# Optimization experiments

Measured on AMD Instinct MI355X. Metric: run time of the kernel, lower is better.

## Reference

```python
import jax, jax.numpy as jnp
import numpy as np
import math

BN_EPS = 1e-5
L2_EPS = 1e-12
TEMPARATURE = 0.01
Q_IN_DIM = 256


def _masked_bn(y, mask, gamma, beta):
    # y: [S, L, D], mask: [S, L] float (1 = valid packed row).
    # Emulates BatchNorm1d (training mode) over the packed valid rows.
    m = mask[..., None]
    cnt = jnp.sum(mask)
    mean = jnp.sum(y * m, axis=(0, 1)) / cnt
    var = jnp.sum(jnp.square(y - mean) * m, axis=(0, 1)) / cnt  # biased var
    return (y - mean) * jax.lax.rsqrt(var + BN_EPS) * gamma + beta


def _ctx_proj(x, W, b, gamma, beta, mask, normalize):
    y = jnp.einsum('sld,od->slo', x, W) + b
    y = jax.nn.relu(_masked_bn(y, mask, gamma, beta))
    if normalize:
        n = jnp.linalg.norm(y, axis=-1, keepdims=True)
        y = y / jnp.maximum(n, L2_EPS)
    return y


def setup_inputs() -> dict:
    key = jax.random.key(0)
    ks = jax.random.split(key, 8)
    S, La, Lb = 256, 128, 512
    Dq, Dkv, Dqk, Dv = 256, 265, 512, 512
    A = jax.random.normal(ks[0], (S, La, Dq), jnp.float32)
    B = jax.random.normal(ks[1], (S, Lb, Dkv), jnp.float32)
    a_lens = jax.random.randint(ks[2], (S,), 1, La + 1, jnp.int32)
    b_lens = jax.random.randint(ks[3], (S,), 1, Lb + 1, jnp.int32)
    pk = jax.random.split(ks[4], 4)
    sc = 0.05
    return {
        'A': A, 'B': B, 'a_lens': a_lens, 'b_lens': b_lens,
        'Wq': sc * jax.random.normal(pk[0], (Dqk, Dq), jnp.float32),
        'bq': jnp.zeros((Dqk,), jnp.float32),
        'gq': jnp.ones((Dqk,), jnp.float32),
        'betaq': jnp.zeros((Dqk,), jnp.float32),
        'Wk': sc * jax.random.normal(pk[1], (Dqk, Dkv), jnp.float32),
        'bk': jnp.zeros((Dqk,), jnp.float32),
        'gk': jnp.ones((Dqk,), jnp.float32),
        'betak': jnp.zeros((Dqk,), jnp.float32),
        'Wv': sc * jax.random.normal(pk[2], (Dv, Dkv), jnp.float32),
        'bv': jnp.zeros((Dv,), jnp.float32),
        'gv': jnp.ones((Dv,), jnp.float32),
        'betav': jnp.zeros((Dv,), jnp.float32),
        'Wf': sc * jax.random.normal(pk[3], (Dq, Dv), jnp.float32),
        'bf': jnp.zeros((Dq,), jnp.float32),
        'gf': jnp.ones((Dq,), jnp.float32),
        'betaf': jnp.zeros((Dq,), jnp.float32),
    }


def reference(A, B, a_lens, b_lens,
              Wq, bq, gq, betaq,
              Wk, bk, gk, betak,
              Wv, bv, gv, betav,
              Wf, bf, gf, betaf):
    S, La, _ = A.shape
    Lb = B.shape[1]
    mask_a = (jnp.arange(La)[None, :] < a_lens[:, None]).astype(A.dtype)  # [S, La]
    mask_b = (jnp.arange(Lb)[None, :] < b_lens[:, None]).astype(B.dtype)  # [S, Lb]

    q = _ctx_proj(A, Wq, bq, gq, betaq, mask_a, True)   # [S, La, Dqk]
    k = _ctx_proj(B, Wk, bk, gk, betak, mask_b, True)   # [S, Lb, Dqk]
    v = _ctx_proj(B, Wv, bv, gv, betav, mask_b, True)   # [S, Lb, Dv]

    scaler = 1.0 / (TEMPARATURE * math.sqrt(Q_IN_DIM))
    scores = jnp.einsum('sad,sbd->sab', q, k) * scaler  # [S, La, Lb]
    scores = jnp.where(mask_b[:, None, :] > 0, scores, -1e30)
    w = jax.nn.softmax(scores, axis=-1)
    wv = jnp.einsum('sab,sbd->sad', w, v)               # [S, La, Dv]

    f = _ctx_proj(wv, Wf, bf, gf, betaf, mask_a, False)  # [S, La, Dq]
    return f * mask_a[..., None]
```

## Files before the change

### kernel.cpp

```cpp
#include <hip/hip_runtime.h>
#include <hip/hip_bf16.h>
#include <stdint.h>


typedef __attribute__((ext_vector_type(8))) short short8;
typedef __attribute__((ext_vector_type(4))) float floatx4;

__device__ __forceinline__ float bf2f(short h) {
    union { unsigned u; float f; } c;
    c.u = ((unsigned)(unsigned short)h) << 16;
    return c.f;
}
__device__ __forceinline__ short f2bf(float f) {
    union { float f; unsigned u; } c;
    c.f = f;
    unsigned u = c.u + 0x7fffu + ((c.u >> 16) & 1u);
    return (short)(u >> 16);
}

__device__ __forceinline__ void async_cp16(const short* g, short* l) {
    __builtin_amdgcn_global_load_lds(
        (const __attribute__((address_space(1))) unsigned int*)g,
        (__attribute__((address_space(3))) unsigned int*)l, 16, 0, 0);
}

__device__ __forceinline__ short8 cvt8load(const float* p) {
    float4 f0 = *(const float4*)(p);
    float4 f1 = *(const float4*)(p + 4);
    short8 r;
    r[0] = f2bf(f0.x); r[1] = f2bf(f0.y); r[2] = f2bf(f0.z); r[3] = f2bf(f0.w);
    r[4] = f2bf(f1.x); r[5] = f2bf(f1.y); r[6] = f2bf(f1.z); r[7] = f2bf(f1.w);
    return r;
}
__device__ __forceinline__ short8 cvt8guard(const float* row, int c0, int Kin) {
    short8 r;
#pragma unroll
    for (int j = 0; j < 8; j++) {
        int c = c0 + j;
        r[j] = (c < Kin) ? f2bf(row[c]) : (short)0;
    }
    return r;
}

__global__ __launch_bounds__(256) void cvt_pad(const float* __restrict__ in,
                                               short* __restrict__ out,
                                               int kin, int kout) {
    long row = blockIdx.x;
    const float* src = in + row * (long)kin;
    short* dst = out + row * (long)kout;
    for (int c = threadIdx.x; c < kout; c += 256)
        dst[c] = (c < kin) ? f2bf(src[c]) : (short)0;
}

__global__ __launch_bounds__(256, 2)
void gemm256(const short* __restrict__ X,
             const short* __restrict__ W0, const short* __restrict__ W1,
             const float* __restrict__ bias0, const float* __restrict__ bias1,
             short* __restrict__ Y0, short* __restrict__ Y1,
             float* __restrict__ st0, float* __restrict__ st1,
             int N, int Kp, const int* __restrict__ lens, int Lshift,
             int nShift, int dual)
{
    __shared__ short SH[(256 + 128) * 96];
    short* At = SH;
    short* Bt = SH + 256 * 96;
    const int lin = blockIdx.x;
    const int xcd = lin & 7, sl = lin >> 3;
    const int nb = sl & ((1 << nShift) - 1);
    const int ms = sl >> nShift;
    const int m0 = (ms * 8 + xcd) * 256;
    int g = 0, n0;
    if (dual) { g = nb & 1; n0 = (nb >> 1) * 128; } else { n0 = nb * 128; }
    const short* W    = g ? W1 : W0;
    const float* bias = g ? bias1 : bias0;
    short* Y          = g ? Y1 : Y0;
    float* stats      = g ? st1 : st0;

    const int tid = threadIdx.x;
    const int l = tid & 63, w = tid >> 6;
    const int quad = l >> 4, l15 = l & 15;
    const int mo = w * 64;

    floatx4 acc[4][8];
#pragma unroll
    for (int i = 0; i < 4; i++)
#pragma unroll
        for (int j = 0; j < 8; j++) acc[i][j] = (floatx4){0.f, 0.f, 0.f, 0.f};

    int offA[12], offB[6];
#pragma unroll
    for (int c = 0; c < 12; c++) {
        unsigned e = c * 2048u + (unsigned)tid * 8u;
        unsigned row = e / 96u;
        unsigned col = e - row * 96u;
        offA[c] = (int)((unsigned)(m0 + row) * (unsigned)Kp + col);
    }
#pragma unroll
    for (int c = 0; c < 6; c++) {
        unsigned e = c * 2048u + (unsigned)tid * 8u;
        unsigned row = e / 96u;
        unsigned col = e - row * 96u;
        offB[c] = (int)((unsigned)(n0 + row) * (unsigned)Kp + col);
    }

    for (int k0 = 0; k0 < Kp; k0 += 96) {
        __syncthreads();
#pragma unroll
        for (int c = 0; c < 12; c++)
            async_cp16(X + offA[c] + k0, At + c * 2048 + tid * 8);
#pragma unroll
        for (int c = 0; c < 6; c++)
            async_cp16(W + offB[c] + k0, Bt + c * 2048 + tid * 8);
        __syncthreads();
#pragma unroll
        for (int seg = 0; seg < 3; seg++) {
            short8 af[4], bfr[8];
#pragma unroll
            for (int i = 0; i < 4; i++)
                af[i] = *(const short8*)(At + (mo + i * 16 + l15) * 96 + seg * 32 + quad * 8);
#pragma unroll
            for (int j = 0; j < 8; j++)
                bfr[j] = *(const short8*)(Bt + (j * 16 + l15) * 96 + seg * 32 + quad * 8);
#pragma unroll
            for (int i = 0; i < 4; i++)
#pragma unroll
                for (int j = 0; j < 8; j++)
                    acc[i][j] = __builtin_amdgcn_mfma_f32_16x16x32_bf16(af[i], bfr[j], acc[i][j], 0, 0, 0);
        }
    }

    __syncthreads();
    const int Lmask = (1 << Lshift) - 1;
    float msk[4][4];
#pragma unroll
    for (int i = 0; i < 4; i++)
#pragma unroll
        for (int r = 0; r < 4; r++) {
            int rg = m0 + mo + i * 16 + quad * 4 + r;
            msk[i][r] = ((rg & Lmask) < lens[rg >> Lshift]) ? 1.f : 0.f;
        }
    short* Cs = SH;
#pragma unroll
    for (int j = 0; j < 8; j++) {
        int coll = j * 16 + l15;
        float bv = bias[n0 + coll];
        float ps = 0.f, pss = 0.f;
#pragma unroll
        for (int i = 0; i < 4; i++)
#pragma unroll
            for (int r = 0; r < 4; r++) {
                int rl = mo + i * 16 + quad * 4 + r;
                float v = acc[i][j][r] + bv;
                Cs[rl * 132 + coll] = f2bf(v);
                ps += v * msk[i][r];
                pss += v * v * msk[i][r];
            }
        ps  += __shfl_xor(ps, 16, 64);  ps  += __shfl_xor(ps, 32, 64);
        pss += __shfl_xor(pss, 16, 64); pss += __shfl_xor(pss, 32, 64);
        if (l < 16) {
            atomicAdd(&stats[n0 + coll], ps);
            atomicAdd(&stats[N + n0 + coll], pss);
        }
    }
    __syncthreads();
#pragma unroll
    for (int c = 0; c < 16; c++) {
        int e = c * 2048 + tid * 8;
        int row = e >> 7, col = e & 127;
        short8 vv = *(const short8*)(Cs + row * 132 + col);
        *(short8*)(Y + (long)(m0 + row) * N + n0 + col) = vv;
    }
}

template<bool XBF16, bool KAL>
__global__ __launch_bounds__(256, 2)
void gemm_bt(const void* __restrict__ Xp, const float* __restrict__ W,
             const float* __restrict__ bias, short* __restrict__ Y,
             int N, int Kin, int Kp, float* __restrict__ stats,
             const int* __restrict__ lens, int Lshift)
{
    __shared__ short At[128 * 32];
    __shared__ short Bt[128 * 32];
    const int m0 = blockIdx.x * 128;
    const int n0 = blockIdx.y * 128;
    const int tid = threadIdx.x;
    const int w = tid >> 6, l = tid & 63;
    const int quad = l >> 4, l15 = l & 15;
    const int mo = (w & 1) * 64, no = (w >> 1) * 64;

    floatx4 acc[4][4];
#pragma unroll
    for (int i = 0; i < 4; i++)
#pragma unroll
        for (int j = 0; j < 4; j++) acc[i][j] = (floatx4){0.f, 0.f, 0.f, 0.f};

    const int srow = tid >> 2;
    const int sc8 = (tid & 3) * 8;

    for (int k0 = 0; k0 < Kp; k0 += 32) {
        __syncthreads();
        const int c0 = k0 + sc8;
        short8 a0, a1, b0, b1;
        if (XBF16) {
            const short* X = (const short*)Xp;
            a0 = *(const short8*)(X + (long)(m0 + srow) * Kp + c0);
            a1 = *(const short8*)(X + (long)(m0 + 64 + srow) * Kp + c0);
        } else {
            const float* X = (const float*)Xp;
            if (KAL) {
                a0 = cvt8load(X + (long)(m0 + srow) * Kin + c0);
                a1 = cvt8load(X + (long)(m0 + 64 + srow) * Kin + c0);
            } else {
                a0 = cvt8guard(X + (long)(m0 + srow) * Kin, c0, Kin);
                a1 = cvt8guard(X + (long)(m0 + 64 + srow) * Kin, c0, Kin);
            }
        }
        if (KAL) {
            b0 = cvt8load(W + (long)(n0 + srow) * Kin + c0);
            b1 = cvt8load(W + (long)(n0 + 64 + srow) * Kin + c0);
        } else {
            b0 = cvt8guard(W + (long)(n0 + srow) * Kin, c0, Kin);
            b1 = cvt8guard(W + (long)(n0 + 64 + srow) * Kin, c0, Kin);
        }
        *(short8*)(At + srow * 32 + sc8) = a0;
        *(short8*)(At + (64 + srow) * 32 + sc8) = a1;
        *(short8*)(Bt + srow * 32 + sc8) = b0;
        *(short8*)(Bt + (64 + srow) * 32 + sc8) = b1;
        __syncthreads();
        short8 af[4], bfr[4];
#pragma unroll
        for (int i = 0; i < 4; i++) {
            af[i]  = *(const short8*)(At + (mo + i * 16 + l15) * 32 + quad * 8);
            bfr[i] = *(const short8*)(Bt + (no + i * 16 + l15) * 32 + quad * 8);
        }
#pragma unroll
        for (int i = 0; i < 4; i++)
#pragma unroll
            for (int j = 0; j < 4; j++)
                acc[i][j] = __builtin_amdgcn_mfma_f32_16x16x32_bf16(af[i], bfr[j], acc[i][j], 0, 0, 0);
    }

    const int Lmask = (1 << Lshift) - 1;
    float msk[4][4];
#pragma unroll
    for (int i = 0; i < 4; i++)
#pragma unroll
        for (int r = 0; r < 4; r++) {
            int rg = m0 + mo + i * 16 + quad * 4 + r;
            msk[i][r] = ((rg & Lmask) < lens[rg >> Lshift]) ? 1.f : 0.f;
        }
#pragma unroll
    for (int j = 0; j < 4; j++) {
        int colj = n0 + no + j * 16 + l15;
        float bv = bias[colj];
        float ps = 0.f, pss = 0.f;
#pragma unroll
        for (int i = 0; i < 4; i++)
#pragma unroll
            for (int r = 0; r < 4; r++) {
                int rg = m0 + mo + i * 16 + quad * 4 + r;
                float v = acc[i][j][r] + bv;
                Y[(long)rg * N + colj] = f2bf(v);
                ps += v * msk[i][r];
                pss += v * v * msk[i][r];
            }
        ps  += __shfl_xor(ps, 16, 64);  ps  += __shfl_xor(ps, 32, 64);
        pss += __shfl_xor(pss, 16, 64); pss += __shfl_xor(pss, 32, 64);
        if (l < 16) {
            atomicAdd(&stats[colj], ps);
            atomicAdd(&stats[N + colj], pss);
        }
    }
}

__global__ void finalize_stats(float* __restrict__ stats, const float* __restrict__ g,
                               const float* __restrict__ beta,
                               const int* __restrict__ lens, int C)
{
    __shared__ int lred[256];
    int t = threadIdx.x;
    if (t < 256) lred[t] = lens[t];
    __syncthreads();
    for (int s2 = 128; s2 > 0; s2 >>= 1) {
        if (t < s2) lred[t] += lred[t + s2];
        __syncthreads();
    }
    float cnt = (float)lred[0];
    if (t < C) {
        float mean = stats[t] / cnt;
        float var = fmaxf(stats[C + t] / cnt - mean * mean, 0.f);
        float a = rsqrtf(var + 1e-5f) * g[t];
        stats[t] = a;
        stats[C + t] = beta[t] - mean * a;
    }
}

__global__ __launch_bounds__(256)
void apply_norm512(short* __restrict__ Y, const float* __restrict__ stats)
{
    int w = threadIdx.x >> 6, l = threadIdx.x & 63;
    long row = (long)blockIdx.x * 4 + w;
    short8 yv = *(const short8*)(Y + row * 512 + l * 8);
    float v[8];
    float ss = 0.f;
#pragma unroll
    for (int i = 0; i < 8; i++) {
        int c = l * 8 + i;
        float t = fmaxf(bf2f(yv[i]) * stats[c] + stats[512 + c], 0.f);
        v[i] = t;
        ss += t * t;
    }
#pragma unroll
    for (int off = 1; off < 64; off <<= 1) ss += __shfl_xor(ss, off, 64);
    float scl = 1.f / fmaxf(sqrtf(ss), 1e-12f);
    short8 o;
#pragma unroll
    for (int i = 0; i < 8; i++) o[i] = f2bf(v[i] * scl);
    *(short8*)(Y + row * 512 + l * 8) = o;
}

__global__ __launch_bounds__(256)
void attention(const short* __restrict__ q, const short* __restrict__ k,
               const short* __restrict__ v, const int* __restrict__ b_lens,
               short* __restrict__ wv, int wvStride)
{
    __shared__ short tile[32 * 520];
    __shared__ short Pscr[4][16 * 40];
    const int lin = blockIdx.x;
    const int xcd = lin & 7, sl = lin >> 3;
    const int a0 = (sl & 1) * 64;
    const int s = (sl >> 1) * 8 + xcd;
    const int tid = threadIdx.x;
    const int w = tid >> 6, l = tid & 63;
    const int quad = l >> 4, l15 = l & 15;
    const int blen = b_lens[s];
    const int sr = tid >> 3;
    const int scg = (tid & 7) * 8;

    short8 qf[16];
    const short* qbase = q + ((long)(s * 128 + a0 + w * 16 + l15)) * 512 + quad * 8;
#pragma unroll
    for (int kk = 0; kk < 16; kk++) qf[kk] = *(const short8*)(qbase + kk * 32);

    floatx4 sc[32];
#pragma unroll
    for (int i = 0; i < 32; i++) sc[i] = (floatx4){0.f, 0.f, 0.f, 0.f};

    const short* kbase = k + (long)s * 512 * 512;
    for (int bt2 = 0; bt2 < 16; ++bt2) {
        __syncthreads();
        const short* krow = kbase + (long)(bt2 * 32 + sr) * 512;
#pragma unroll
        for (int i = 0; i < 2; i++) {
            short8 t0 = *(const short8*)(krow + i * 256 + scg);
            short8 t1 = *(const short8*)(krow + i * 256 + 64 + scg);
            short8 t2 = *(const short8*)(krow + i * 256 + 128 + scg);
            short8 t3 = *(const short8*)(krow + i * 256 + 192 + scg);
            *(short8*)(&tile[sr * 520 + i * 256 + scg]) = t0;
            *(short8*)(&tile[sr * 520 + i * 256 + 64 + scg]) = t1;
            *(short8*)(&tile[sr * 520 + i * 256 + 128 + scg]) = t2;
            *(short8*)(&tile[sr * 520 + i * 256 + 192 + scg]) = t3;
        }
        __syncthreads();
#pragma unroll
        for (int kk = 0; kk < 16; kk++) {
            short8 f0 = *(const short8*)(&tile[l15 * 520 + kk * 32 + quad * 8]);
            short8 f1 = *(const short8*)(&tile[(16 + l15) * 520 + kk * 32 + quad * 8]);
            sc[bt2 * 2]     = __builtin_amdgcn_mfma_f32_16x16x32_bf16(qf[kk], f0, sc[bt2 * 2], 0, 0, 0);
            sc[bt2 * 2 + 1] = __builtin_amdgcn_mfma_f32_16x16x32_bf16(qf[kk], f1, sc[bt2 * 2 + 1], 0, 0, 0);
        }
    }

    const float scaler = 6.25f;
    float mrow[4] = {-__builtin_inff(), -__builtin_inff(), -__builtin_inff(), -__builtin_inff()};
#pragma unroll
    for (int bt = 0; bt < 32; ++bt) {
        bool valid = (bt * 16 + l15) < blen;
#pragma unroll
        for (int r = 0; r < 4; r++) {
            float v2 = valid ? sc[bt][r] * scaler : -__builtin_inff();
            sc[bt][r] = v2;
            mrow[r] = fmaxf(mrow[r], v2);
        }
    }
#pragma unroll
    for (int r = 0; r < 4; r++) {
#pragma unroll
        for (int off = 1; off < 16; off <<= 1)
            mrow[r] = fmaxf(mrow[r], __shfl_xor(mrow[r], off, 64));
    }
    float ssum[4] = {0.f, 0.f, 0.f, 0.f};
#pragma unroll
    for (int bt = 0; bt < 32; ++bt)
#pragma unroll
        for (int r = 0; r < 4; r++) {
            float p = __expf(sc[bt][r] - mrow[r]);
            sc[bt][r] = p;
            ssum[r] += p;
        }
#pragma unroll
    for (int r = 0; r < 4; r++) {
#pragma unroll
        for (int off = 1; off < 16; off <<= 1) ssum[r] += __shfl_xor(ssum[r], off, 64);
        ssum[r] = 1.f / ssum[r];
    }

    short8 pf[16];
    short* Pw = Pscr[w];
#pragma unroll
    for (int kk = 0; kk < 16; kk++) {
#pragma unroll
        for (int half = 0; half < 2; half++)
#pragma unroll
            for (int r = 0; r < 4; r++)
                Pw[(quad * 4 + r) * 40 + half * 16 + l15] = f2bf(sc[kk * 2 + half][r] * ssum[r]);
        pf[kk] = *(const short8*)(&Pw[l15 * 40 + quad * 8]);
    }

    const short* vbase = v + (long)s * 512 * 512;
    short* wvbase = wv + (long)(s * 128 + a0 + w * 16 + quad * 4) * wvStride;
    for (int dt = 0; dt < 16; ++dt) {
        __syncthreads();
#pragma unroll
        for (int round = 0; round < 2; round++) {
            int b = round * 256 + tid;
            const short* vr = vbase + (long)b * 512 + dt * 32;
            short8 x0 = *(const short8*)(vr);
            short8 x1 = *(const short8*)(vr + 8);
            short8 x2 = *(const short8*)(vr + 16);
            short8 x3 = *(const short8*)(vr + 24);
#pragma unroll
            for (int j = 0; j < 8; j++) {
                tile[j * 520 + b]        = x0[j];
                tile[(8 + j) * 520 + b]  = x1[j];
                tile[(16 + j) * 520 + b] = x2[j];
                tile[(24 + j) * 520 + b] = x3[j];
            }
        }
        __syncthreads();
        floatx4 o0 = (floatx4){0.f, 0.f, 0.f, 0.f};
        floatx4 o1 = (floatx4){0.f, 0.f, 0.f, 0.f};
#pragma unroll
        for (int kk = 0; kk < 16; kk++) {
            short8 f0 = *(const short8*)(&tile[l15 * 520 + kk * 32 + quad * 8]);
            short8 f1 = *(const short8*)(&tile[(16 + l15) * 520 + kk * 32 + quad * 8]);
            o0 = __builtin_amdgcn_mfma_f32_16x16x32_bf16(pf[kk], f0, o0, 0, 0, 0);
            o1 = __builtin_amdgcn_mfma_f32_16x16x32_bf16(pf[kk], f1, o1, 0, 0, 0);
        }
#pragma unroll
        for (int r = 0; r < 4; r++) {
            wvbase[(long)r * wvStride + dt * 32 + l15]      = f2bf(o0[r]);
            wvbase[(long)r * wvStride + dt * 32 + 16 + l15] = f2bf(o1[r]);
        }
    }

    if (wvStride > 512) {
        int r = tid >> 2, cb = (tid & 3) * 16;
        short8 z = (short8){0, 0, 0, 0, 0, 0, 0, 0};
        short* pz = wv + (long)(s * 128 + a0 + r) * wvStride + 512 + cb;
        *(short8*)(pz) = z;
        *(short8*)(pz + 8) = z;
    }
}

__global__ __launch_bounds__(256)
void apply_f(const short* __restrict__ Yf, const float* __restrict__ stats,
             const int* __restrict__ a_lens, float* __restrict__ out)
{
    const long total = (long)32768 * 256;
    for (long e = (long)blockIdx.x * 256 + threadIdx.x; e < total; e += (long)gridDim.x * 256) {
        int c = (int)(e & 255);
        long row = e >> 8;
        int sI = (int)(row >> 7), pos = (int)(row & 127);
        float v = fmaxf(bf2f(Yf[e]) * stats[c] + stats[256 + c], 0.f);
        out[e] = (pos < a_lens[sI]) ? v : 0.f;
    }
}

extern "C" void kernel_launch(void* const* d_in, const int* in_sizes, int n_in,
                              void* d_out, int out_size, void* d_ws, size_t ws_size,
                              hipStream_t stream)
{
    (void)in_sizes; (void)n_in; (void)out_size;
    const float* A     = (const float*)d_in[0];
    const float* B     = (const float*)d_in[1];
    const int* a_lens  = (const int*)d_in[2];
    const int* b_lens  = (const int*)d_in[3];
    const float* Wq    = (const float*)d_in[4];
    const float* bq    = (const float*)d_in[5];
    const float* gq    = (const float*)d_in[6];
    const float* betaq = (const float*)d_in[7];
    const float* Wk    = (const float*)d_in[8];
    const float* bk    = (const float*)d_in[9];
    const float* gk    = (const float*)d_in[10];
    const float* betak = (const float*)d_in[11];
    const float* Wv    = (const float*)d_in[12];
    const float* bv    = (const float*)d_in[13];
    const float* gv    = (const float*)d_in[14];
    const float* betav = (const float*)d_in[15];
    const float* Wf    = (const float*)d_in[16];
    const float* bfp   = (const float*)d_in[17];
    const float* gf    = (const float*)d_in[18];
    const float* betaf = (const float*)d_in[19];
    float* out = (float*)d_out;
    char* base = (char*)d_ws;

    const size_t oWqb = 0;
    const size_t oWkb = oWqb + 294912;
    const size_t oWvb = oWkb + 294912;
    const size_t oWfb = oWvb + 294912;
    const size_t oBbf = oWfb + 294912;
    const size_t oQb  = oBbf + 75497472;
    const size_t oYv  = oQb + 33554432;
    const size_t oKb  = oYv + 134217728;
    const size_t oSt  = oKb + 134217728;
    const size_t FAST_NEED = oSt + 16384;

    if (ws_size >= FAST_NEED) {
        short* Wqb = (short*)(base + oWqb);
        short* Wkb = (short*)(base + oWkb);
        short* Wvb = (short*)(base + oWvb);
        short* Wfb = (short*)(base + oWfb);
        short* Bbf = (short*)(base + oBbf);
        short* qb  = (short*)(base + oQb);
        short* Yv  = (short*)(base + oYv);
        short* kb  = (short*)(base + oKb);
        short* Abf = (short*)(base + oKb);
        short* wvb = (short*)(base + oBbf);
        short* Yf  = (short*)(base + oQb);
        float* stQ = (float*)(base + oSt);
        float* stK = stQ + 1024;
        float* stV = stQ + 2048;
        float* stF = stQ + 3072;

        hipMemsetAsync(stQ, 0, 16384, stream);

        cvt_pad<<<32768, 256, 0, stream>>>(A, Abf, 256, 288);
        cvt_pad<<<131072, 256, 0, stream>>>(B, Bbf, 265, 288);
        cvt_pad<<<512, 256, 0, stream>>>(Wq, Wqb, 256, 288);
        cvt_pad<<<512, 256, 0, stream>>>(Wk, Wkb, 265, 288);
        cvt_pad<<<512, 256, 0, stream>>>(Wv, Wvb, 265, 288);
        cvt_pad<<<256, 256, 0, stream>>>(Wf, Wfb, 512, 576);

        gemm256<<<512, 256, 0, stream>>>(
            Abf, Wqb, Wqb, bq, bq, qb, qb, stQ, stQ, 512, 288, a_lens, 7, 2, 0);
        gemm256<<<4096, 256, 0, stream>>>(
            Bbf, Wvb, Wkb, bv, bk, Yv, kb, stV, stK, 512, 288, b_lens, 9, 3, 1);

        finalize_stats<<<1, 512, 0, stream>>>(stV, gv, betav, b_lens, 512);
        finalize_stats<<<1, 512, 0, stream>>>(stK, gk, betak, b_lens, 512);
        finalize_stats<<<1, 512, 0, stream>>>(stQ, gq, betaq, a_lens, 512);
        apply_norm512<<<32768, 256, 0, stream>>>(Yv, stV);
        apply_norm512<<<32768, 256, 0, stream>>>(kb, stK);
        apply_norm512<<<8192, 256, 0, stream>>>(qb, stQ);

        attention<<<512, 256, 0, stream>>>(qb, kb, Yv, b_lens, wvb, 576);

        gemm256<<<256, 256, 0, stream>>>(
            wvb, Wfb, Wfb, bfp, bfp, Yf, Yf, stF, stF, 256, 576, a_lens, 7, 1, 0);
        finalize_stats<<<1, 512, 0, stream>>>(stF, gf, betaf, a_lens, 256);
        apply_f<<<8192, 256, 0, stream>>>(Yf, stF, a_lens, out);
        return;
    }

    short* qb  = (short*)(base);
    short* Yv  = (short*)(base + 33554432);
    short* kb  = (short*)(base + 33554432 + 134217728);
    short* wvb = (short*)(base + 33554432 + 2L * 134217728);
    float* stQ = (float*)(base + 2L * 33554432 + 2L * 134217728);
    float* stK = stQ + 1024;
    float* stV = stQ + 2048;
    float* stF = stQ + 3072;
    short* Yf  = qb;

    hipMemsetAsync(stQ, 0, 16384, stream);

    gemm_bt<false, true><<<dim3(256, 4), 256, 0, stream>>>(
        A, Wq, bq, qb, 512, 256, 256, stQ, a_lens, 7);
    gemm_bt<false, false><<<dim3(1024, 4), 256, 0, stream>>>(
        B, Wv, bv, Yv, 512, 265, 288, stV, b_lens, 9);
    finalize_stats<<<1, 512, 0, stream>>>(stV, gv, betav, b_lens, 512);
    apply_norm512<<<32768, 256, 0, stream>>>(Yv, stV);
    gemm_bt<false, false><<<dim3(1024, 4), 256, 0, stream>>>(
        B, Wk, bk, kb, 512, 265, 288, stK, b_lens, 9);
    finalize_stats<<<1, 512, 0, stream>>>(stK, gk, betak, b_lens, 512);
    apply_norm512<<<32768, 256, 0, stream>>>(kb, stK);
    finalize_stats<<<1, 512, 0, stream>>>(stQ, gq, betaq, a_lens, 512);
    apply_norm512<<<8192, 256, 0, stream>>>(qb, stQ);
    attention<<<512, 256, 0, stream>>>(qb, kb, Yv, b_lens, wvb, 512);
    gemm_bt<true, true><<<dim3(256, 2), 256, 0, stream>>>(
        wvb, Wf, bfp, Yf, 256, 512, 512, stF, a_lens, 7);
    finalize_stats<<<1, 512, 0, stream>>>(stF, gf, betaf, a_lens, 256);
    apply_f<<<8192, 256, 0, stream>>>(Yf, stF, a_lens, out);
}
```

Before: 857.1 us.

## Double-buffer gemm256 K-loop with 32-wide stages and two-pass epilogue staging

Replaces the single-buffered 96-wide K tile loop in gemm256 with a double-buffered 32-wide pipeline, so async global-to-LDS loads for the next step are issued while MFMAs run on the current buffer, with one barrier per step. Shared memory shrinks from 384x96 to 24576 shorts, which may help occupancy. Because the smaller LDS cannot hold the full 256x128 output tile, the epilogue now writes it in two 128-row passes through LDS. The trade-off is more loop iterations and barriers, plus extra synchronisation in the epilogue.

Result: no change. 859.3 us (+0.2%).

```diff
diff --git a/kernel.cpp b/kernel.cpp
--- a/kernel.cpp
+++ b/kernel.cpp
@@ -61,9 +61,7 @@
              int N, int Kp, const int* __restrict__ lens, int Lshift,
              int nShift, int dual)
 {
-    __shared__ short SH[(256 + 128) * 96];
-    short* At = SH;
-    short* Bt = SH + 256 * 96;
+    __shared__ short SH[24576];
     const int lin = blockIdx.x;
     const int xcd = lin & 7, sl = lin >> 3;
     const int nb = sl & ((1 << nShift) - 1);
@@ -87,49 +85,57 @@
 #pragma unroll
         for (int j = 0; j < 8; j++) acc[i][j] = (floatx4){0.f, 0.f, 0.f, 0.f};
 
-    int offA[12], offB[6];
-#pragma unroll
-    for (int c = 0; c < 12; c++) {
-        unsigned e = c * 2048u + (unsigned)tid * 8u;
-        unsigned row = e / 96u;
-        unsigned col = e - row * 96u;
-        offA[c] = (int)((unsigned)(m0 + row) * (unsigned)Kp + col);
-    }
-#pragma unroll
-    for (int c = 0; c < 6; c++) {
-        unsigned e = c * 2048u + (unsigned)tid * 8u;
-        unsigned row = e / 96u;
-        unsigned col = e - row * 96u;
-        offB[c] = (int)((unsigned)(n0 + row) * (unsigned)Kp + col);
-    }
-
-    for (int k0 = 0; k0 < Kp; k0 += 96) {
-        __syncthreads();
-#pragma unroll
-        for (int c = 0; c < 12; c++)
-            async_cp16(X + offA[c] + k0, At + c * 2048 + tid * 8);
-#pragma unroll
-        for (int c = 0; c < 6; c++)
-            async_cp16(W + offB[c] + k0, Bt + c * 2048 + tid * 8);
-        __syncthreads();
-#pragma unroll
-        for (int seg = 0; seg < 3; seg++) {
-            short8 af[4], bfr[8];
-#pragma unroll
-            for (int i = 0; i < 4; i++)
-                af[i] = *(const short8*)(At + (mo + i * 16 + l15) * 96 + seg * 32 + quad * 8);
+    const int srow = tid >> 2;
+    const int scol = (tid & 3) * 8;
+    const short* Xs = X + (long)(m0 + srow) * Kp + scol;
+    const short* Ws = W + (long)(n0 + srow) * Kp + scol;
+    const long strideA = (long)64 * Kp;
+    const int nsteps = Kp >> 5;
+
+    {
+        short* At = SH;
+        short* Bt = SH + 8192;
+#pragma unroll
+        for (int c = 0; c < 4; c++)
+            async_cp16(Xs + c * strideA, At + c * 2048 + tid * 8);
+#pragma unroll
+        for (int c = 0; c < 2; c++)
+            async_cp16(Ws + c * strideA, Bt + c * 2048 + tid * 8);
+    }
+    __syncthreads();
+
+    int cur = 0;
+    for (int t = 0; t < nsteps; t++) {
+        if (t + 1 < nsteps) {
+            short* At = SH + (cur ^ 1) * 12288;
+            short* Bt = At + 8192;
+            const short* Xk = Xs + (t + 1) * 32;
+            const short* Wk = Ws + (t + 1) * 32;
+#pragma unroll
+            for (int c = 0; c < 4; c++)
+                async_cp16(Xk + c * strideA, At + c * 2048 + tid * 8);
+#pragma unroll
+            for (int c = 0; c < 2; c++)
+                async_cp16(Wk + c * strideA, Bt + c * 2048 + tid * 8);
+        }
+        const short* At = SH + cur * 12288;
+        const short* Bt = At + 8192;
+        short8 af[4], bfr[8];
+#pragma unroll
+        for (int i = 0; i < 4; i++)
+            af[i] = *(const short8*)(At + (mo + i * 16 + l15) * 32 + quad * 8);
+#pragma unroll
+        for (int j = 0; j < 8; j++)
+            bfr[j] = *(const short8*)(Bt + (j * 16 + l15) * 32 + quad * 8);
+#pragma unroll
+        for (int i = 0; i < 4; i++)
 #pragma unroll
             for (int j = 0; j < 8; j++)
-                bfr[j] = *(const short8*)(Bt + (j * 16 + l15) * 96 + seg * 32 + quad * 8);
-#pragma unroll
-            for (int i = 0; i < 4; i++)
-#pragma unroll
-                for (int j = 0; j < 8; j++)
-                    acc[i][j] = __builtin_amdgcn_mfma_f32_16x16x32_bf16(af[i], bfr[j], acc[i][j], 0, 0, 0);
-        }
-    }
-
-    __syncthreads();
+                acc[i][j] = __builtin_amdgcn_mfma_f32_16x16x32_bf16(af[i], bfr[j], acc[i][j], 0, 0, 0);
+        __syncthreads();
+        cur ^= 1;
+    }
+
     const int Lmask = (1 << Lshift) - 1;
     float msk[4][4];
 #pragma unroll
@@ -139,36 +145,52 @@
             int rg = m0 + mo + i * 16 + quad * 4 + r;
             msk[i][r] = ((rg & Lmask) < lens[rg >> Lshift]) ? 1.f : 0.f;
         }
-    short* Cs = SH;
+    float bv[8];
+#pragma unroll
+    for (int j = 0; j < 8; j++) bv[j] = bias[n0 + j * 16 + l15];
+
 #pragma unroll
     for (int j = 0; j < 8; j++) {
-        int coll = j * 16 + l15;
-        float bv = bias[n0 + coll];
         float ps = 0.f, pss = 0.f;
 #pragma unroll
         for (int i = 0; i < 4; i++)
 #pragma unroll
             for (int r = 0; r < 4; r++) {
-                int rl = mo + i * 16 + quad * 4 + r;
-                float v = acc[i][j][r] + bv;
-                Cs[rl * 132 + coll] = f2bf(v);
+                float v = acc[i][j][r] + bv[j];
                 ps += v * msk[i][r];
                 pss += v * v * msk[i][r];
             }
         ps  += __shfl_xor(ps, 16, 64);  ps  += __shfl_xor(ps, 32, 64);
         pss += __shfl_xor(pss, 16, 64); pss += __shfl_xor(pss, 32, 64);
         if (l < 16) {
-            atomicAdd(&stats[n0 + coll], ps);
-            atomicAdd(&stats[N + n0 + coll], pss);
-        }
-    }
-    __syncthreads();
-#pragma unroll
-    for (int c = 0; c < 16; c++) {
-        int e = c * 2048 + tid * 8;
-        int row = e >> 7, col = e & 127;
-        short8 vv = *(const short8*)(Cs + row * 132 + col);
-        *(short8*)(Y + (long)(m0 + row) * N + n0 + col) = vv;
+            atomicAdd(&stats[n0 + j * 16 + l15], ps);
+            atomicAdd(&stats[N + n0 + j * 16 + l15], pss);
+        }
+    }
+
+    short* Cs = SH;
+#pragma unroll
+    for (int pass = 0; pass < 2; pass++) {
+        __syncthreads();
+        if ((w >> 1) == pass) {
+            const int mol = (w & 1) * 64;
+#pragma unroll
+            for (int j = 0; j < 8; j++)
+#pragma unroll
+                for (int i = 0; i < 4; i++)
+#pragma unroll
+                    for (int r = 0; r < 4; r++)
+                        Cs[(mol + i * 16 + quad * 4 + r) * 132 + j * 16 + l15] =
+                            f2bf(acc[i][j][r] + bv[j]);
+        }
+        __syncthreads();
+#pragma unroll
+        for (int c = 0; c < 8; c++) {
+            int e = c * 2048 + tid * 8;
+            int row = e >> 7, col = e & 127;
+            short8 vv = *(const short8*)(Cs + row * 132 + col);
+            *(short8*)(Y + (long)(m0 + pass * 128 + row) * N + n0 + col) = vv;
+        }
     }
 }
 
@@ -252,14 +274,14 @@
 #pragma unroll
     for (int j = 0; j < 4; j++) {
         int colj = n0 + no + j * 16 + l15;
-        float bv = bias[colj];
+        float bvs = bias[colj];
         float ps = 0.f, pss = 0.f;
 #pragma unroll
         for (int i = 0; i < 4; i++)
 #pragma unroll
             for (int r = 0; r < 4; r++) {
                 int rg = m0 + mo + i * 16 + quad * 4 + r;
-                float v = acc[i][j][r] + bv;
+                float v = acc[i][j][r] + bvs;
                 Y[(long)rg * N + colj] = f2bf(v);
                 ps += v * msk[i][r];
                 pss += v * v * msk[i][r];
```
